# Optimization experiments

Hardware: AMD Instinct MI355X
Metric: run time of the kernel (lower is better)

Reference implementation:

```python
import jax, jax.numpy as jnp
import numpy as np

B, T, D, H = 2, 2048, 1024, 16
HD = D // H  # 64
THETA = 10000.0


def _rope(x, pos):
    # x: (B,H,T,HD), pos: (T,) int
    half = HD // 2
    inv_freq = THETA ** (-jnp.arange(half, dtype=jnp.float32) * 2.0 / HD)  # (half,)
    ang = pos.astype(jnp.float32)[:, None] * inv_freq[None, :]  # (T, half)
    cos = jnp.cos(ang)[None, None]  # (1,1,T,half)
    sin = jnp.sin(ang)[None, None]
    x1 = x[..., 0::2]
    x2 = x[..., 1::2]
    r1 = x1 * cos - x2 * sin
    r2 = x1 * sin + x2 * cos
    return jnp.stack([r1, r2], axis=-1).reshape(x.shape)


def setup_inputs() -> dict:
    key = jax.random.key(0)
    ks = jax.random.split(key, 9)
    s = 0.02
    inp = {
        "x": jax.random.normal(ks[0], (B, T, D), dtype=jnp.float32),
        "token_positions": jnp.arange(T, dtype=jnp.int64),
        "wq": jax.random.normal(ks[1], (D, D), dtype=jnp.float32) * s,
        "bq": jnp.zeros((D,), dtype=jnp.float32),
        "wk": jax.random.normal(ks[2], (D, D), dtype=jnp.float32) * s,
        "bk": jnp.zeros((D,), dtype=jnp.float32),
        "wv": jax.random.normal(ks[3], (D, D), dtype=jnp.float32) * s,
        "bv": jnp.zeros((D,), dtype=jnp.float32),
        "wo": jax.random.normal(ks[4], (D, D), dtype=jnp.float32) * s,
        "bo": jnp.zeros((D,), dtype=jnp.float32),
    }
    return inp


def reference(x, token_positions, wq, bq, wk, bk, wv, bv, wo, bo):
    # Linear projections (torch Linear: x @ W.T + b)
    q = x @ wq.T + bq
    k = x @ wk.T + bk
    v = x @ wv.T + bv
    # (B,T,D) -> (B,H,T,HD)
    q = q.reshape(B, T, H, HD).transpose(0, 2, 1, 3)
    k = k.reshape(B, T, H, HD).transpose(0, 2, 1, 3)
    v = v.reshape(B, T, H, HD).transpose(0, 2, 1, 3)
    # RoPE on q and k
    q = _rope(q, token_positions)
    k = _rope(k, token_positions)
    # causal masked softmax attention
    scores = jnp.einsum('bhqd,bhkd->bhqk', q, k) / jnp.sqrt(jnp.float32(HD))
    keep = jnp.tril(jnp.ones((T, T), dtype=bool))  # keep mask (True = attend)
    scores = jnp.where(keep[None, None], scores, -jnp.inf)
    probs = jax.nn.softmax(scores, axis=-1)
    out = jnp.einsum('bhqk,bhkd->bhqd', probs, v)
    out = out.transpose(0, 2, 1, 3).reshape(B, T, D)
    return out @ wo.T + bo
```

## Files before the change

### kernel.cpp

```cpp
#include <hip/hip_runtime.h>
#include <hip/hip_bf16.h>

#define Bc 2
#define Tc 2048
#define Dc 1024
#define Hc 16
#define HDc 64

typedef __attribute__((ext_vector_type(4))) float f32x4;
typedef __attribute__((ext_vector_type(4))) short short4v;
typedef __attribute__((ext_vector_type(8))) short short8;
typedef __bf16 bf16x8 __attribute__((ext_vector_type(8)));

static __device__ __forceinline__ short f2bf(float f) {
  union { float f; unsigned u; } v; v.f = f;
  unsigned r = v.u + 0x7fffu + ((v.u >> 16) & 1u);
  return (short)(r >> 16);
}

static __device__ __forceinline__ f32x4 mfma16(bf16x8 a, bf16x8 b, f32x4 c) {
  return __builtin_amdgcn_mfma_f32_16x16x32_bf16(a, b, c, 0, 0, 0);
}

__global__ __launch_bounds__(256) void wconv_kernel(
    const float* __restrict__ wq, const float* __restrict__ wk,
    const float* __restrict__ wv, short* __restrict__ Wb)
{
  const int z = blockIdx.y;
  const float* src = (z == 0) ? wq : (z == 1) ? wk : wv;
  const size_t i = ((size_t)blockIdx.x * 256 + threadIdx.x) * 8;
  const float4 a0 = *(const float4*)(src + i);
  const float4 a1 = *(const float4*)(src + i + 4);
  short8 r;
  r[0] = f2bf(a0.x); r[1] = f2bf(a0.y); r[2] = f2bf(a0.z); r[3] = f2bf(a0.w);
  r[4] = f2bf(a1.x); r[5] = f2bf(a1.y); r[6] = f2bf(a1.z); r[7] = f2bf(a1.w);
  *(short8*)(Wb + (size_t)z * 1048576 + i) = r;
}

__global__ __launch_bounds__(256) void rope_tab_kernel(
    const int* __restrict__ tp, float2* __restrict__ tab)
{
  const int idx = blockIdx.x * 256 + threadIdx.x;
  const int t = idx >> 5, i = idx & 31;
  const float inv = expf((float)i * -0.2878231366242557f);
  float sn, cs;
  sincosf((float)tp[t] * inv, &sn, &cs);
  tab[idx] = make_float2(cs, sn);
}

__global__ __launch_bounds__(256) void qkv_kernel(
    const float* __restrict__ x, const short* __restrict__ Wb,
    const float* __restrict__ bq, const float* __restrict__ bk,
    const float* __restrict__ bv, const float2* __restrict__ rtab,
    short* __restrict__ Qw, short* __restrict__ Kw, short* __restrict__ Vw)
{
  __shared__ short As[64][40];
  __shared__ short Bs[3][64][40];
  const int tid = threadIdx.x, lane = tid & 63, w = tid >> 6;
  const int wr = w >> 1, wc = w & 1;
  const int nbase = blockIdx.x * 64, mbase = blockIdx.y * 64;
  const int srow = tid >> 2, scol = (tid & 3) * 8;
  const int fr = lane & 15, fq = lane >> 4, kg = fq * 8;

  f32x4 acc[3][2][2] = {};

  for (int k0 = 0; k0 < Dc; k0 += 32) {
    if (k0) __syncthreads();
    {
      const float* src = x + (size_t)(mbase + srow) * Dc + k0 + scol;
      const float4 a0 = *(const float4*)src;
      const float4 a1 = *(const float4*)(src + 4);
      short* dst = &As[srow][scol];
      dst[0] = f2bf(a0.x); dst[1] = f2bf(a0.y); dst[2] = f2bf(a0.z); dst[3] = f2bf(a0.w);
      dst[4] = f2bf(a1.x); dst[5] = f2bf(a1.y); dst[6] = f2bf(a1.z); dst[7] = f2bf(a1.w);
    }
#pragma unroll
    for (int z = 0; z < 3; ++z)
      *(short8*)&Bs[z][srow][scol] =
          *(const short8*)(Wb + (size_t)z * 1048576 + (size_t)(nbase + srow) * Dc + k0 + scol);
    __syncthreads();
    const bf16x8 af0 = *(const bf16x8*)&As[wr * 32 + fr][kg];
    const bf16x8 af1 = *(const bf16x8*)&As[wr * 32 + 16 + fr][kg];
#pragma unroll
    for (int z = 0; z < 3; ++z) {
      const bf16x8 b0 = *(const bf16x8*)&Bs[z][wc * 32 + fr][kg];
      const bf16x8 b1 = *(const bf16x8*)&Bs[z][wc * 32 + 16 + fr][kg];
      acc[z][0][0] = mfma16(af0, b0, acc[z][0][0]);
      acc[z][0][1] = mfma16(af0, b1, acc[z][0][1]);
      acc[z][1][0] = mfma16(af1, b0, acc[z][1][0]);
      acc[z][1][1] = mfma16(af1, b1, acc[z][1][1]);
    }
  }

#pragma unroll
  for (int a2 = 0; a2 < 2; ++a2)
#pragma unroll
    for (int b2 = 0; b2 < 2; ++b2) {
      const int n = nbase + wc * 32 + b2 * 16 + fr;
      const float bi0 = bq[n], bi1 = bk[n], bi2 = bv[n];
      const int hd = n & 63, h = n >> 6;
      const int mb = mbase + wr * 32 + a2 * 16 + fq * 4;
      const int tb = mb & (Tc - 1);
      const int bbi = mb >> 11;
      short4v pv;
#pragma unroll
      for (int r = 0; r < 4; ++r) {
        const int t = tb + r;
        const size_t oidx = (((size_t)bbi * Hc + h) * Tc + t) * HDc + hd;
        const float2 cs = rtab[t * 32 + (hd >> 1)];
        float v0 = acc[0][a2][b2][r] + bi0;
        float v1 = acc[1][a2][b2][r] + bi1;
        const float n0 = __shfl_xor(v0, 1);
        const float n1 = __shfl_xor(v1, 1);
        v0 = (hd & 1) ? (n0 * cs.y + v0 * cs.x) : (v0 * cs.x - n0 * cs.y);
        v1 = (hd & 1) ? (n1 * cs.y + v1 * cs.x) : (v1 * cs.x - n1 * cs.y);
        Qw[oidx] = f2bf(v0);
        Kw[oidx] = f2bf(v1);
        pv[r] = f2bf(acc[2][a2][b2][r] + bi2);
      }
      *(short4v*)(Vw + ((size_t)(bbi * Hc + h) * HDc + hd) * Tc + tb) = pv;
    }
}

__global__ __launch_bounds__(256) void out_kernel(
    const short* __restrict__ Ob, const float* __restrict__ wo,
    const float* __restrict__ bo, float* __restrict__ out)
{
  __shared__ short As[64][40];
  __shared__ short Bs[64][40];
  const int tid = threadIdx.x, lane = tid & 63, w = tid >> 6;
  const int wr = w >> 1, wc = w & 1;
  const int nbase = blockIdx.x * 64, mbase = blockIdx.y * 64;
  const int srow = tid >> 2, scol = (tid & 3) * 8;
  const int fr = lane & 15, fq = lane >> 4, kg = fq * 8;

  f32x4 acc[2][2] = {};

  for (int k0 = 0; k0 < Dc; k0 += 32) {
    if (k0) __syncthreads();
    *(short8*)&As[srow][scol] = *(const short8*)(Ob + (size_t)(mbase + srow) * Dc + k0 + scol);
    {
      const float* src = wo + (size_t)(nbase + srow) * Dc + k0 + scol;
      const float4 b0 = *(const float4*)src;
      const float4 b1 = *(const float4*)(src + 4);
      short* dst = &Bs[srow][scol];
      dst[0] = f2bf(b0.x); dst[1] = f2bf(b0.y); dst[2] = f2bf(b0.z); dst[3] = f2bf(b0.w);
      dst[4] = f2bf(b1.x); dst[5] = f2bf(b1.y); dst[6] = f2bf(b1.z); dst[7] = f2bf(b1.w);
    }
    __syncthreads();
    const bf16x8 af0 = *(const bf16x8*)&As[wr * 32 + fr][kg];
    const bf16x8 af1 = *(const bf16x8*)&As[wr * 32 + 16 + fr][kg];
    const bf16x8 b0 = *(const bf16x8*)&Bs[wc * 32 + fr][kg];
    const bf16x8 b1 = *(const bf16x8*)&Bs[wc * 32 + 16 + fr][kg];
    acc[0][0] = mfma16(af0, b0, acc[0][0]);
    acc[0][1] = mfma16(af0, b1, acc[0][1]);
    acc[1][0] = mfma16(af1, b0, acc[1][0]);
    acc[1][1] = mfma16(af1, b1, acc[1][1]);
  }

#pragma unroll
  for (int a2 = 0; a2 < 2; ++a2)
#pragma unroll
    for (int b2 = 0; b2 < 2; ++b2) {
      const int n = nbase + wc * 32 + b2 * 16 + fr;
      const float bv = bo[n];
#pragma unroll
      for (int r = 0; r < 4; ++r) {
        const int m = mbase + wr * 32 + a2 * 16 + fq * 4 + r;
        out[(size_t)m * Dc + n] = acc[a2][b2][r] + bv;
      }
    }
}

__global__ __launch_bounds__(64) void attn_kernel(
    const short* __restrict__ Qw, const short* __restrict__ Kw,
    const short* __restrict__ Vtg, short* __restrict__ Ob)
{
  __shared__ short Ps[16][72];
  const int lane = threadIdx.x;
  const int bh = blockIdx.y, bb = bh >> 4, h = bh & 15;
  const int qt = (int)gridDim.x - 1 - blockIdx.x;
  const int q16 = qt * 16;
  const size_t baseQ = (size_t)bh * Tc * HDc;
  const size_t baseV = (size_t)bh * HDc * Tc;
  const int fr = lane & 15, fq = lane >> 4, kg = fq * 8;

  bf16x8 qf0, qf1;
  {
    const short* qrow = Qw + baseQ + (size_t)(q16 + fr) * HDc;
    qf0 = *(const bf16x8*)(qrow + kg);
    qf1 = *(const bf16x8*)(qrow + 32 + kg);
  }

  f32x4 o[4] = {};
  float mrun[4] = {-1e30f, -1e30f, -1e30f, -1e30f};
  float lrun[4] = {0.f, 0.f, 0.f, 0.f};

  const int ntiles = (qt >> 2) + 1;
  for (int kt = 0; kt < ntiles; ++kt) {
    const int kv0 = kt * 64;
    f32x4 s[4];
#pragma unroll
    for (int cf = 0; cf < 4; ++cf) {
      const short* kr = Kw + baseQ + (size_t)(kv0 + cf * 16 + fr) * HDc + kg;
      f32x4 acc = {};
      acc = mfma16(qf0, *(const bf16x8*)kr, acc);
      acc = mfma16(qf1, *(const bf16x8*)(kr + 32), acc);
      s[cf] = acc * 0.125f;
    }
    bf16x8 vb[2][4];
#pragma unroll
    for (int ks = 0; ks < 2; ++ks)
#pragma unroll
      for (int df = 0; df < 4; ++df)
        vb[ks][df] = *(const bf16x8*)(Vtg + baseV + (size_t)(df * 16 + fr) * Tc + kv0 + ks * 32 + kg);

    if (kt == ntiles - 1) {
#pragma unroll
      for (int cf = 0; cf < 4; ++cf) {
        const int col = kv0 + cf * 16 + fr;
#pragma unroll
        for (int r = 0; r < 4; ++r)
          if (col > q16 + fq * 4 + r) s[cf][r] = -1e30f;
      }
    }
    float pm[4];
#pragma unroll
    for (int r = 0; r < 4; ++r)
      pm[r] = fmaxf(fmaxf(s[0][r], s[1][r]), fmaxf(s[2][r], s[3][r]));
#pragma unroll
    for (int d = 1; d < 16; d <<= 1)
#pragma unroll
      for (int r = 0; r < 4; ++r)
        pm[r] = fmaxf(pm[r], __shfl_xor(pm[r], d));
    float alpha[4], rs[4];
#pragma unroll
    for (int r = 0; r < 4; ++r) {
      const float mn = fmaxf(mrun[r], pm[r]);
      alpha[r] = __expf(mrun[r] - mn);
      mrun[r] = mn;
      rs[r] = 0.f;
    }
#pragma unroll
    for (int cf = 0; cf < 4; ++cf)
#pragma unroll
      for (int r = 0; r < 4; ++r) {
        const float p = __expf(s[cf][r] - mrun[r]);
        s[cf][r] = p;
        rs[r] += p;
      }
#pragma unroll
    for (int d = 1; d < 16; d <<= 1)
#pragma unroll
      for (int r = 0; r < 4; ++r)
        rs[r] += __shfl_xor(rs[r], d);
#pragma unroll
    for (int r = 0; r < 4; ++r)
      lrun[r] = lrun[r] * alpha[r] + rs[r];
#pragma unroll
    for (int df = 0; df < 4; ++df)
#pragma unroll
      for (int r = 0; r < 4; ++r)
        o[df][r] *= alpha[r];
#pragma unroll
    for (int cf = 0; cf < 4; ++cf)
#pragma unroll
      for (int r = 0; r < 4; ++r)
        Ps[fq * 4 + r][cf * 16 + fr] = f2bf(s[cf][r]);
#pragma unroll
    for (int ks = 0; ks < 2; ++ks) {
      const bf16x8 pa = *(const bf16x8*)&Ps[fr][ks * 32 + kg];
#pragma unroll
      for (int df = 0; df < 4; ++df)
        o[df] = mfma16(pa, vb[ks][df], o[df]);
    }
  }

#pragma unroll
  for (int df = 0; df < 4; ++df)
#pragma unroll
    for (int r = 0; r < 4; ++r) {
      const int t = q16 + fq * 4 + r;
      const float val = o[df][r] / lrun[r];
      Ob[((size_t)bb * Tc + t) * Dc + h * HDc + df * 16 + fr] = f2bf(val);
    }
}

extern "C" void kernel_launch(void* const* d_in, const int* in_sizes, int n_in,
                              void* d_out, int out_size, void* d_ws, size_t ws_size,
                              hipStream_t stream) {
  const float* x  = (const float*)d_in[0];
  const int*   tp = (const int*)d_in[1];
  const float* wq = (const float*)d_in[2];
  const float* bq = (const float*)d_in[3];
  const float* wk = (const float*)d_in[4];
  const float* bk = (const float*)d_in[5];
  const float* wv = (const float*)d_in[6];
  const float* bv = (const float*)d_in[7];
  const float* wo = (const float*)d_in[8];
  const float* bo = (const float*)d_in[9];
  float* out = (float*)d_out;

  char* ws = (char*)d_ws;
  short* Qw = (short*)(ws);
  short* Kw = (short*)(ws + (8u << 20));
  short* Vw = (short*)(ws + (16u << 20));
  short* Ob = (short*)(ws + (24u << 20));
  short*  Wb   = (short*)(ws + (24u << 20));
  float2* rtab = (float2*)(ws + (30u << 20));

  dim3 blk(256);
  wconv_kernel<<<dim3(512, 3), blk, 0, stream>>>(wq, wk, wv, Wb);
  rope_tab_kernel<<<dim3(256), blk, 0, stream>>>(tp, rtab);
  qkv_kernel<<<dim3(16, 64), blk, 0, stream>>>(x, Wb, bq, bk, bv, rtab, Qw, Kw, Vw);
  attn_kernel<<<dim3(128, 32), dim3(64), 0, stream>>>(Qw, Kw, Vw, Ob);
  out_kernel<<<dim3(16, 64), blk, 0, stream>>>(Ob, wo, bo, out);
}
```

Before: 339.0 us.

## Process two 16-row query tiles per attention wave to reuse K/V loads

Each attention wavefront now handles 32 query rows as two 16-row fragments instead of 16 rows. K and V tiles loaded from global memory are shared across both fragments, which halves K/V traffic per query row. The grid shrinks from 128 to 64 blocks along the query axis. In exchange it roughly doubles register use per wave, lowers the number of waves available to hide latency, and adds extra masked work on the diagonal tile.

```diff
diff --git a/kernel.cpp b/kernel.cpp
--- a/kernel.cpp
+++ b/kernel.cpp
@@ -176,37 +176,39 @@
     const short* __restrict__ Qw, const short* __restrict__ Kw,
     const short* __restrict__ Vtg, short* __restrict__ Ob)
 {
-  __shared__ short Ps[16][72];
+  __shared__ short Ps[2][16][72];
   const int lane = threadIdx.x;
   const int bh = blockIdx.y, bb = bh >> 4, h = bh & 15;
-  const int qt = (int)gridDim.x - 1 - blockIdx.x;
-  const int q16 = qt * 16;
+  const int j = (int)gridDim.x - 1 - blockIdx.x;
+  const int q32 = j * 32;
   const size_t baseQ = (size_t)bh * Tc * HDc;
   const size_t baseV = (size_t)bh * HDc * Tc;
   const int fr = lane & 15, fq = lane >> 4, kg = fq * 8;
 
-  bf16x8 qf0, qf1;
-  {
-    const short* qrow = Qw + baseQ + (size_t)(q16 + fr) * HDc;
-    qf0 = *(const bf16x8*)(qrow + kg);
-    qf1 = *(const bf16x8*)(qrow + 32 + kg);
+  bf16x8 qf[2][2];
+#pragma unroll
+  for (int f = 0; f < 2; ++f) {
+    const short* qrow = Qw + baseQ + (size_t)(q32 + f * 16 + fr) * HDc;
+    qf[f][0] = *(const bf16x8*)(qrow + kg);
+    qf[f][1] = *(const bf16x8*)(qrow + 32 + kg);
   }
 
-  f32x4 o[4] = {};
-  float mrun[4] = {-1e30f, -1e30f, -1e30f, -1e30f};
-  float lrun[4] = {0.f, 0.f, 0.f, 0.f};
-
-  const int ntiles = (qt >> 2) + 1;
+  f32x4 o[2][4] = {};
+  float mrun[2][4], lrun[2][4];
+#pragma unroll
+  for (int f = 0; f < 2; ++f)
+#pragma unroll
+    for (int r = 0; r < 4; ++r) { mrun[f][r] = -1e30f; lrun[f][r] = 0.f; }
+
+  const int ntiles = (j >> 1) + 1;
   for (int kt = 0; kt < ntiles; ++kt) {
     const int kv0 = kt * 64;
-    f32x4 s[4];
+    bf16x8 ka[4][2];
 #pragma unroll
     for (int cf = 0; cf < 4; ++cf) {
       const short* kr = Kw + baseQ + (size_t)(kv0 + cf * 16 + fr) * HDc + kg;
-      f32x4 acc = {};
-      acc = mfma16(qf0, *(const bf16x8*)kr, acc);
-      acc = mfma16(qf1, *(const bf16x8*)(kr + 32), acc);
-      s[cf] = acc * 0.125f;
+      ka[cf][0] = *(const bf16x8*)kr;
+      ka[cf][1] = *(const bf16x8*)(kr + 32);
     }
     bf16x8 vb[2][4];
 #pragma unroll
@@ -215,75 +217,108 @@
       for (int df = 0; df < 4; ++df)
         vb[ks][df] = *(const bf16x8*)(Vtg + baseV + (size_t)(df * 16 + fr) * Tc + kv0 + ks * 32 + kg);
 
+    f32x4 s[2][4];
+#pragma unroll
+    for (int f = 0; f < 2; ++f)
+#pragma unroll
+      for (int cf = 0; cf < 4; ++cf) {
+        f32x4 acc = {};
+        acc = mfma16(qf[f][0], ka[cf][0], acc);
+        acc = mfma16(qf[f][1], ka[cf][1], acc);
+        s[f][cf] = acc * 0.125f;
+      }
+
     if (kt == ntiles - 1) {
 #pragma unroll
-      for (int cf = 0; cf < 4; ++cf) {
-        const int col = kv0 + cf * 16 + fr;
+      for (int f = 0; f < 2; ++f)
+#pragma unroll
+        for (int cf = 0; cf < 4; ++cf) {
+          const int col = kv0 + cf * 16 + fr;
+#pragma unroll
+          for (int r = 0; r < 4; ++r)
+            if (col > q32 + f * 16 + fq * 4 + r) s[f][cf][r] = -1e30f;
+        }
+    }
+
+    float pm[2][4], alpha[2][4], rs[2][4];
+#pragma unroll
+    for (int f = 0; f < 2; ++f)
+#pragma unroll
+      for (int r = 0; r < 4; ++r)
+        pm[f][r] = fmaxf(fmaxf(s[f][0][r], s[f][1][r]), fmaxf(s[f][2][r], s[f][3][r]));
+#pragma unroll
+    for (int d = 1; d < 16; d <<= 1)
+#pragma unroll
+      for (int f = 0; f < 2; ++f)
 #pragma unroll
         for (int r = 0; r < 4; ++r)
-          if (col > q16 + fq * 4 + r) s[cf][r] = -1e30f;
-      }
-    }
-    float pm[4];
-#pragma unroll
-    for (int r = 0; r < 4; ++r)
-      pm[r] = fmaxf(fmaxf(s[0][r], s[1][r]), fmaxf(s[2][r], s[3][r]));
+          pm[f][r] = fmaxf(pm[f][r], __shfl_xor(pm[f][r], d));
+#pragma unroll
+    for (int f = 0; f < 2; ++f)
+#pragma unroll
+      for (int r = 0; r < 4; ++r) {
+        const float mn = fmaxf(mrun[f][r], pm[f][r]);
+        alpha[f][r] = __expf(mrun[f][r] - mn);
+        mrun[f][r] = mn;
+        rs[f][r] = 0.f;
+      }
+#pragma unroll
+    for (int f = 0; f < 2; ++f)
+#pragma unroll
+      for (int cf = 0; cf < 4; ++cf)
+#pragma unroll
+        for (int r = 0; r < 4; ++r) {
+          const float p = __expf(s[f][cf][r] - mrun[f][r]);
+          s[f][cf][r] = p;
+          rs[f][r] += p;
+        }
 #pragma unroll
     for (int d = 1; d < 16; d <<= 1)
 #pragma unroll
+      for (int f = 0; f < 2; ++f)
+#pragma unroll
+        for (int r = 0; r < 4; ++r)
+          rs[f][r] += __shfl_xor(rs[f][r], d);
+#pragma unroll
+    for (int f = 0; f < 2; ++f)
+#pragma unroll
       for (int r = 0; r < 4; ++r)
-        pm[r] = fmaxf(pm[r], __shfl_xor(pm[r], d));
-    float alpha[4], rs[4];
-#pragma unroll
-    for (int r = 0; r < 4; ++r) {
-      const float mn = fmaxf(mrun[r], pm[r]);
-      alpha[r] = __expf(mrun[r] - mn);
-      mrun[r] = mn;
-      rs[r] = 0.f;
-    }
-#pragma unroll
-    for (int cf = 0; cf < 4; ++cf)
+        lrun[f][r] = lrun[f][r] * alpha[f][r] + rs[f][r];
+#pragma unroll
+    for (int f = 0; f < 2; ++f)
+#pragma unroll
+      for (int df = 0; df < 4; ++df)
+#pragma unroll
+        for (int r = 0; r < 4; ++r)
+          o[f][df][r] *= alpha[f][r];
+#pragma unroll
+    for (int f = 0; f < 2; ++f)
+#pragma unroll
+      for (int cf = 0; cf < 4; ++cf)
+#pragma unroll
+        for (int r = 0; r < 4; ++r)
+          Ps[f][fq * 4 + r][cf * 16 + fr] = f2bf(s[f][cf][r]);
+#pragma unroll
+    for (int f = 0; f < 2; ++f)
+#pragma unroll
+      for (int ks = 0; ks < 2; ++ks) {
+        const bf16x8 pa = *(const bf16x8*)&Ps[f][fr][ks * 32 + kg];
+#pragma unroll
+        for (int df = 0; df < 4; ++df)
+          o[f][df] = mfma16(pa, vb[ks][df], o[f][df]);
+      }
+  }
+
+#pragma unroll
+  for (int f = 0; f < 2; ++f)
+#pragma unroll
+    for (int df = 0; df < 4; ++df)
 #pragma unroll
       for (int r = 0; r < 4; ++r) {
-        const float p = __expf(s[cf][r] - mrun[r]);
-        s[cf][r] = p;
-        rs[r] += p;
-      }
-#pragma unroll
-    for (int d = 1; d < 16; d <<= 1)
-#pragma unroll
-      for (int r = 0; r < 4; ++r)
-        rs[r] += __shfl_xor(rs[r], d);
-#pragma unroll
-    for (int r = 0; r < 4; ++r)
-      lrun[r] = lrun[r] * alpha[r] + rs[r];
-#pragma unroll
-    for (int df = 0; df < 4; ++df)
-#pragma unroll
-      for (int r = 0; r < 4; ++r)
-        o[df][r] *= alpha[r];
-#pragma unroll
-    for (int cf = 0; cf < 4; ++cf)
-#pragma unroll
-      for (int r = 0; r < 4; ++r)
-        Ps[fq * 4 + r][cf * 16 + fr] = f2bf(s[cf][r]);
-#pragma unroll
-    for (int ks = 0; ks < 2; ++ks) {
-      const bf16x8 pa = *(const bf16x8*)&Ps[fr][ks * 32 + kg];
-#pragma unroll
-      for (int df = 0; df < 4; ++df)
-        o[df] = mfma16(pa, vb[ks][df], o[df]);
-    }
-  }
-
-#pragma unroll
-  for (int df = 0; df < 4; ++df)
-#pragma unroll
-    for (int r = 0; r < 4; ++r) {
-      const int t = q16 + fq * 4 + r;
-      const float val = o[df][r] / lrun[r];
-      Ob[((size_t)bb * Tc + t) * Dc + h * HDc + df * 16 + fr] = f2bf(val);
-    }
+        const int t = q32 + f * 16 + fq * 4 + r;
+        Ob[((size_t)bb * Tc + t) * Dc + h * HDc + df * 16 + fr] =
+            f2bf(o[f][df][r] / lrun[f][r]);
+      }
 }
 
 extern "C" void kernel_launch(void* const* d_in, const int* in_sizes, int n_in,
@@ -313,6 +348,6 @@
   wconv_kernel<<<dim3(512, 3), blk, 0, stream>>>(wq, wk, wv, Wb);
   rope_tab_kernel<<<dim3(256), blk, 0, stream>>>(tp, rtab);
   qkv_kernel<<<dim3(16, 64), blk, 0, stream>>>(x, Wb, bq, bk, bv, rtab, Qw, Kw, Vw);
-  attn_kernel<<<dim3(128, 32), dim3(64), 0, stream>>>(Qw, Kw, Vw, Ob);
+  attn_kernel<<<dim3(64, 32), dim3(64), 0, stream>>>(Qw, Kw, Vw, Ob);
   out_kernel<<<dim3(16, 64), blk, 0, stream>>>(Ob, wo, bo, out);
 }
```

New measurement: 284.1 us. 16.2% less time.
